# Kernel optimization log

Hardware: AMD Instinct MI355X
Metric: run time of the kernel (lower is better)

## Reference

```python
import jax, jax.numpy as jnp
import numpy as np

N, D_TOK, K = 8192, 256, 16


def knn_idx(xyz, k):
    # squared pairwise distances, diagonal excluded (loop=False)
    sq = jnp.sum(xyz * xyz, axis=-1)                      # [N]
    dist = sq[:, None] - 2.0 * (xyz @ xyz.T) + sq[None, :]  # [N,N]
    dist = dist + jnp.eye(xyz.shape[0], dtype=xyz.dtype) * jnp.asarray(1e10, xyz.dtype)
    _, idx = jax.lax.top_k(-dist, k)                      # [N,k] nearest neighbors j for each target i
    return idx


def edgeconv(x, nbr, W1, b1, W2, b2):
    # EdgeConv message: nn(concat(x_i, x_j - x_i)), aggr = max over neighbors
    n, d = x.shape
    k = nbr.shape[1]
    xi = x[:, None, :]                                    # [N,1,D]
    xj = x[nbr]                                           # [N,k,D] gather
    msg = jnp.concatenate([jnp.broadcast_to(xi, (n, k, d)), xj - xi], axis=-1)  # [N,k,2D]
    h = jax.nn.relu(msg @ W1 + b1) @ W2 + b2              # [N,k,token_dim]
    return jnp.max(h, axis=1)                             # [N,token_dim]


def setup_inputs() -> dict:
    key = jax.random.key(0)
    ks = jax.random.split(key, 10)
    d_in = 2 * (D_TOK + 3)
    s1 = 1.0 / np.sqrt(d_in)
    s2 = 1.0 / np.sqrt(D_TOK)
    return {
        "xyz": jax.random.normal(ks[0], (N, 3), dtype=jnp.float32),
        "feat": jax.random.normal(ks[1], (N, D_TOK), dtype=jnp.float32),
        "W1a": jax.random.normal(ks[2], (d_in, D_TOK), dtype=jnp.float32) * s1,
        "b1a": jnp.zeros((D_TOK,), dtype=jnp.float32),
        "W2a": jax.random.normal(ks[3], (D_TOK, D_TOK), dtype=jnp.float32) * s2,
        "b2a": jnp.zeros((D_TOK,), dtype=jnp.float32),
        "W1b": jax.random.normal(ks[4], (d_in, D_TOK), dtype=jnp.float32) * s1,
        "b1b": jnp.zeros((D_TOK,), dtype=jnp.float32),
        "W2b": jax.random.normal(ks[5], (D_TOK, D_TOK), dtype=jnp.float32) * s2,
        "b2b": jnp.zeros((D_TOK,), dtype=jnp.float32),
    }


def reference(xyz, feat, W1a, b1a, W2a, b2a, W1b, b1b, W2b, b2b):
    nbr = knn_idx(xyz, K)                                 # [N,k], built once, reused by both convs
    x = jnp.concatenate([feat, xyz], axis=-1)             # [N, D_TOK+3]
    x = edgeconv(x, nbr, W1a, b1a, W2a, b2a)              # [N, D_TOK]
    x = jnp.concatenate([x, xyz], axis=-1)                # [N, D_TOK+3]
    x = edgeconv(x, nbr, W1b, b1b, W2b, b2b)              # [N, D_TOK]
    return x
```

## Files before the change

### kernel.cpp

```cpp
#include <hip/hip_runtime.h>
#include <cfloat>

#define N_PTS 8192
#define DTOK 256
#define KNN 16

typedef __attribute__((ext_vector_type(8))) short short8;
typedef __attribute__((ext_vector_type(4))) float float4v;
typedef __attribute__((ext_vector_type(2))) float float2v;

__device__ inline short f2bf(float f) {
  unsigned u = __float_as_uint(f);
  u += 0x7fffu + ((u >> 16) & 1u);
  return (short)(u >> 16);
}
__device__ inline float bf2f(short h) {
  return __uint_as_float(((unsigned)(unsigned short)h) << 16);
}

__device__ inline float2v pk_mul(float2v a, float2v b) {
  float2v d;
  asm("v_pk_mul_f32 %0, %1, %2" : "=v"(d) : "v"(a), "v"(b));
  return d;
}
__device__ inline float2v pk_fma(float2v a, float2v b, float2v c) {
  float2v d;
  asm("v_pk_fma_f32 %0, %1, %2, %3" : "=v"(d) : "v"(a), "v"(b), "v"(c));
  return d;
}
__device__ inline float2v pk_add(float2v a, float2v b) {
  float2v d;
  asm("v_pk_add_f32 %0, %1, %2" : "=v"(d) : "v"(a), "v"(b));
  return d;
}

__global__ __launch_bounds__(256) void knn_prep_kernel(
    const float* __restrict__ xyz, float4* __restrict__ xyz4) {
  const int i = blockIdx.x * 256 + threadIdx.x;
  float x = xyz[3 * i], y = xyz[3 * i + 1], z = xyz[3 * i + 2];
  float sq = __fadd_rn(__fadd_rn(__fmul_rn(x, x), __fmul_rn(y, y)),
                       __fmul_rn(z, z));
  xyz4[i] = make_float4(x, y, z, sq);
}

__device__ inline void insert_group(float d, int base, float t, int lane,
                                    float& sd, int& sj, float& s15) {
  unsigned long long m = __ballot(d <= t);
  while (m) {
    const int src = __ffsll(m) - 1;
    m &= m - 1;
    const float dc = __shfl(d, src);
    if (dc < s15) {
      const int jc = base + src;
      const unsigned long long bm = __ballot(sd <= dc) & 0xFFFFull;
      const int pos = (int)__popcll(bm);
      const float pu = __shfl_up(sd, 1);
      const int ju = __shfl_up(sj, 1);
      if (lane < 16) {
        if (lane > pos)        { sd = pu; sj = ju; }
        else if (lane == pos)  { sd = dc; sj = jc; }
      }
      s15 = __shfl(sd, 15);
    }
  }
}

#define KCH 512
#define NCH (N_PTS / KCH)
#define QPW 4

__global__ __launch_bounds__(256) void knn_select_kernel(
    const float4* __restrict__ xyz4, int* __restrict__ nbr) {
  __shared__ float4 sA[2][4][64];
  __shared__ float4 sB[2][4][64];
  const int tid = threadIdx.x;
  const int lane = tid & 63;
  const int wave = tid >> 6;
  const int ibase = blockIdx.x * (4 * QPW) + wave * QPW;

  float2v qx[QPW], qy[QPW], qz[QPW], qs[QPW];
  #pragma unroll
  for (int q = 0; q < QPW; ++q) {
    const float4 p = xyz4[ibase + q];
    qx[q] = (float2v){p.x, p.x};
    qy[q] = (float2v){p.y, p.y};
    qz[q] = (float2v){p.z, p.z};
    qs[q] = (float2v){p.w, p.w};
  }
  const float2v n2 = {-2.0f, -2.0f};

  const int ib128 = ibase & ~127;
  int ihh[QPW], ill[QPW];
  #pragma unroll
  for (int q = 0; q < QPW; ++q) {
    ihh[q] = ((ibase + q) >> 6) & 1;
    ill[q] = (ibase + q) & 63;
  }

  const int sgj = wave * 128 + lane;

  {
    const float4 c0 = xyz4[sgj];
    const float4 c1 = xyz4[sgj + 64];
    sA[0][wave][lane] = make_float4(c0.x, c1.x, c0.y, c1.y);
    sB[0][wave][lane] = make_float4(c0.z, c1.z, c0.w, c1.w);
  }
  __syncthreads();

  float am0[QPW], am1[QPW];
  #pragma unroll
  for (int q = 0; q < QPW; ++q) { am0[q] = FLT_MAX; am1[q] = FLT_MAX; }

  for (int c = 0; c < NCH; ++c) {
    const int b = c & 1;
    float4 nx0, nx1;
    if (c < NCH - 1) {
      nx0 = xyz4[(c + 1) * KCH + sgj];
      nx1 = xyz4[(c + 1) * KCH + sgj + 64];
    }
    const int cbase = c * KCH;
    #pragma unroll
    for (int ps = 0; ps < 4; ++ps) {
      const float4 a = sA[b][ps][lane];
      const float4 bb = sB[b][ps][lane];
      const float2v px = {a.x, a.y}, py = {a.z, a.w};
      const float2v pz = {bb.x, bb.y}, pw = {bb.z, bb.w};
      const bool selfg = (cbase + ps * 128 == ib128);
      #pragma unroll
      for (int q = 0; q < QPW; ++q) {
        const float2v dot =
            pk_fma(qz[q], pz, pk_fma(qy[q], py, pk_mul(qx[q], px)));
        float2v d = pk_add(pk_fma(n2, dot, qs[q]), pw);
        if (selfg) {
          if (lane == ill[q]) {
            if (ihh[q]) d.y = __fadd_rn(d.y, 1e10f);
            else        d.x = __fadd_rn(d.x, 1e10f);
          }
        }
        am0[q] = fminf(am0[q], d.x);
        am1[q] = fminf(am1[q], d.y);
      }
    }
    if (c < NCH - 1) {
      sA[b ^ 1][wave][lane] = make_float4(nx0.x, nx1.x, nx0.y, nx1.y);
      sB[b ^ 1][wave][lane] = make_float4(nx0.z, nx1.z, nx0.w, nx1.w);
    }
    __syncthreads();
  }

  float v[QPW];
  #pragma unroll
  for (int q = 0; q < QPW; ++q) v[q] = fminf(am0[q], am1[q]);
  #pragma unroll
  for (int k = 2; k <= 64; k <<= 1) {
    #pragma unroll
    for (int j = k >> 1; j > 0; j >>= 1) {
      const bool keepmin = ((lane & k) == 0) == ((lane & j) == 0);
      #pragma unroll
      for (int q = 0; q < QPW; ++q) {
        const float o = __shfl_xor(v[q], j, 64);
        v[q] = keepmin ? fminf(v[q], o) : fmaxf(v[q], o);
      }
    }
  }
  float t[QPW];
  #pragma unroll
  for (int q = 0; q < QPW; ++q)
    t[q] = __shfl(v[q], 15, 64);

  float sd[QPW], s15[QPW];
  int sj[QPW];
  #pragma unroll
  for (int q = 0; q < QPW; ++q) {
    sd[q] = FLT_MAX; s15[q] = FLT_MAX; sj[q] = 0;
  }

  {
    const float4 c0 = xyz4[sgj];
    const float4 c1 = xyz4[sgj + 64];
    sA[0][wave][lane] = make_float4(c0.x, c1.x, c0.y, c1.y);
    sB[0][wave][lane] = make_float4(c0.z, c1.z, c0.w, c1.w);
  }
  __syncthreads();

  for (int c = 0; c < NCH; ++c) {
    const int b = c & 1;
    float4 nx0, nx1;
    if (c < NCH - 1) {
      nx0 = xyz4[(c + 1) * KCH + sgj];
      nx1 = xyz4[(c + 1) * KCH + sgj + 64];
    }
    const int cbase = c * KCH;

    #pragma unroll
    for (int ps = 0; ps < 4; ++ps) {
      const float4 a = sA[b][ps][lane];
      const float4 bb = sB[b][ps][lane];
      const float2v px = {a.x, a.y}, py = {a.z, a.w};
      const float2v pz = {bb.x, bb.y}, pw = {bb.z, bb.w};
      const int base = cbase + ps * 128;
      const bool selfg = (base == ib128);
      float2v dd[QPW];
      #pragma unroll
      for (int q = 0; q < QPW; ++q) {
        const float2v dot =
            pk_fma(qz[q], pz, pk_fma(qy[q], py, pk_mul(qx[q], px)));
        dd[q] = pk_add(pk_fma(n2, dot, qs[q]), pw);
        if (selfg) {
          if (lane == ill[q]) {
            if (ihh[q]) dd[q].y = __fadd_rn(dd[q].y, 1e10f);
            else        dd[q].x = __fadd_rn(dd[q].x, 1e10f);
          }
        }
      }
      #pragma unroll
      for (int q = 0; q < QPW; ++q) {
        insert_group(dd[q].x, base,      t[q], lane, sd[q], sj[q], s15[q]);
        insert_group(dd[q].y, base + 64, t[q], lane, sd[q], sj[q], s15[q]);
      }
    }

    if (c < NCH - 1) {
      sA[b ^ 1][wave][lane] = make_float4(nx0.x, nx1.x, nx0.y, nx1.y);
      sB[b ^ 1][wave][lane] = make_float4(nx0.z, nx1.z, nx0.w, nx1.w);
    }
    __syncthreads();
  }
  if (lane < 16) {
    #pragma unroll
    for (int q = 0; q < QPW; ++q)
      nbr[(ibase + q) * KNN + lane] = sj[q];
  }
}

__global__ __launch_bounds__(256) void convert_w_kernel(
    const float* __restrict__ W1, short* __restrict__ bhi,
    short* __restrict__ blo) {
  const int n = blockIdx.x;
  const int k = threadIdx.x;
  const float v = (n < 256) ? W1[k * DTOK + n]
                            : W1[(259 + k) * DTOK + (n - 256)];
  short h = f2bf(v);
  bhi[n * 256 + k] = h;
  blo[n * 256 + k] = f2bf(v - bf2f(h));
}

__global__ __launch_bounds__(256, 2) void pq_gemm_fused_kernel(
    const float* __restrict__ A, const short* __restrict__ Bthi,
    const short* __restrict__ Btlo, const float* __restrict__ xyz,
    const float* __restrict__ W1, const float* __restrict__ b1,
    float* __restrict__ R, float* __restrict__ Q) {
  __shared__ short Ahi[64][32], Alo[64][32];
  __shared__ short Bhi[128][32], Blo[128][32];
  __shared__ float Qs[64][65];
  __shared__ float sx[64][3];
  __shared__ float swz[6][64];
  __shared__ float sb1[64];

  const int tid = threadIdx.x;
  const int lane = tid & 63;
  const int wave = tid >> 6;
  const int l15 = lane & 15;
  const int quad = lane >> 4;
  const int mh = wave & 1;
  const int qh = wave >> 1;
  const int m0 = blockIdx.x * 64;
  const int np0 = blockIdx.y * 64;

  if (tid < 64) {
    sx[tid][0] = xyz[(m0 + tid) * 3];
    sx[tid][1] = xyz[(m0 + tid) * 3 + 1];
    sx[tid][2] = xyz[(m0 + tid) * 3 + 2];
  } else if (tid < 128) {
    int n = tid - 64;
    sb1[n] = b1[np0 + n];
    #pragma unroll
    for (int r = 0; r < 3; ++r) {
      swz[r][n] = W1[(256 + r) * DTOK + np0 + n];
      swz[3 + r][n] = W1[(515 + r) * DTOK + np0 + n];
    }
  }

  float4v acc[2][4];
  #pragma unroll
  for (int mf = 0; mf < 2; ++mf)
    #pragma unroll
    for (int nf = 0; nf < 4; ++nf)
      #pragma unroll
      for (int e = 0; e < 4; ++e) acc[mf][nf][e] = 0.f;

  const int ar = tid >> 2;
  const int ak = (tid & 3) * 8;

  #pragma unroll 1
  for (int kc = 0; kc < 8; ++kc) {
    const int k0 = kc * 32;
    __syncthreads();
    {
      const float* asrc = A + (size_t)(m0 + ar) * 256 + k0 + ak;
      float4 a0 = *(const float4*)asrc;
      float4 a1 = *(const float4*)(asrc + 4);
      float v[8] = {a0.x, a0.y, a0.z, a0.w, a1.x, a1.y, a1.z, a1.w};
      short8 h8, l8;
      #pragma unroll
      for (int e = 0; e < 8; ++e) {
        short h = f2bf(v[e]);
        h8[e] = h;
        l8[e] = f2bf(v[e] - bf2f(h));
      }
      *(short8*)(&Ahi[ar][ak]) = h8;
      *(short8*)(&Alo[ar][ak]) = l8;
    }
    #pragma unroll
    for (int l = 0; l < 4; ++l) {
      const int rem = tid + 256 * (l & 1);
      const int row = rem >> 2;
      const int koff = (rem & 3) * 8;
      const int n = (row < 64) ? (np0 + row) : (256 + np0 + row - 64);
      const short* src = ((l < 2) ? Bthi : Btlo) + (size_t)n * 256 + k0 + koff;
      short8 vv = *(const short8*)src;
      if (l < 2) *(short8*)(&Bhi[row][koff]) = vv;
      else       *(short8*)(&Blo[row][koff]) = vv;
    }
    __syncthreads();

    short8 ah[2], al[2], bh[4], bl[4];
    #pragma unroll
    for (int mf = 0; mf < 2; ++mf) {
      ah[mf] = *(const short8*)(&Ahi[mh * 32 + mf * 16 + l15][quad * 8]);
      al[mf] = *(const short8*)(&Alo[mh * 32 + mf * 16 + l15][quad * 8]);
    }
    #pragma unroll
    for (int nf = 0; nf < 4; ++nf) {
      bh[nf] = *(const short8*)(&Bhi[qh * 64 + nf * 16 + l15][quad * 8]);
      bl[nf] = *(const short8*)(&Blo[qh * 64 + nf * 16 + l15][quad * 8]);
    }
    #pragma unroll
    for (int mf = 0; mf < 2; ++mf)
      #pragma unroll
      for (int nf = 0; nf < 4; ++nf) {
        acc[mf][nf] = __builtin_amdgcn_mfma_f32_16x16x32_bf16(
            ah[mf], bh[nf], acc[mf][nf], 0, 0, 0);
        acc[mf][nf] = __builtin_amdgcn_mfma_f32_16x16x32_bf16(
            ah[mf], bl[nf], acc[mf][nf], 0, 0, 0);
        acc[mf][nf] = __builtin_amdgcn_mfma_f32_16x16x32_bf16(
            al[mf], bh[nf], acc[mf][nf], 0, 0, 0);
      }
  }

  if (qh == 1) {
    #pragma unroll
    for (int mf = 0; mf < 2; ++mf)
      #pragma unroll
      for (int nf = 0; nf < 4; ++nf)
        #pragma unroll
        for (int e = 0; e < 4; ++e) {
          int row = mh * 32 + mf * 16 + quad * 4 + e;
          int col = nf * 16 + l15;
          float q = acc[mf][nf][e] + sx[row][0] * swz[3][col] +
                    sx[row][1] * swz[4][col] + sx[row][2] * swz[5][col];
          Qs[row][col] = q;
          Q[(size_t)(m0 + row) * DTOK + np0 + col] = q;
        }
  }
  __syncthreads();
  if (qh == 0) {
    #pragma unroll
    for (int mf = 0; mf < 2; ++mf)
      #pragma unroll
      for (int nf = 0; nf < 4; ++nf)
        #pragma unroll
        for (int e = 0; e < 4; ++e) {
          int row = mh * 32 + mf * 16 + quad * 4 + e;
          int col = nf * 16 + l15;
          float p = acc[mf][nf][e] + sx[row][0] * swz[0][col] +
                    sx[row][1] * swz[1][col] + sx[row][2] * swz[2][col];
          R[(size_t)(m0 + row) * DTOK + np0 + col] =
              (p + sb1[col]) - Qs[row][col];
        }
  }
}

#define EP 8

__global__ __launch_bounds__(256, 2) void edge_mfma_kernel(
    const float* __restrict__ R, const float* __restrict__ Q,
    const int* __restrict__ nbr, const float* __restrict__ W2,
    const float* __restrict__ b2, float* __restrict__ out,
    int num_groups, int groups_per_block) {
  __shared__ short Hs[EP * KNN * DTOK];
  const int lane = threadIdx.x & 63;
  const int wave = threadIdx.x >> 6;
  const int l15 = lane & 15;
  const int quad = lane >> 4;

  short8 bfr[4][8];
  #pragma unroll
  for (int nt_i = 0; nt_i < 4; ++nt_i) {
    const int n = (wave * 4 + nt_i) * 16 + l15;
    #pragma unroll
    for (int kt = 0; kt < 8; ++kt) {
      short8 f;
      #pragma unroll
      for (int jj = 0; jj < 8; ++jj) {
        int k = kt * 32 + quad * 8 + jj;
        f[jj] = f2bf(W2[k * DTOK + n]);
      }
      bfr[nt_i][kt] = f;
    }
  }

  const int wc8 = lane >> 1;
  const int wsub = (lane & 1) * 4;

  for (int gi = 0; gi < groups_per_block; ++gi) {
    const int g = blockIdx.x + gi * gridDim.x;
    if (g >= num_groups) break;
    const int i0 = g * EP;

    {
      const int ia = i0 + wave * 2;
      const int jr0 = nbr[ia * KNN + l15];
      const int jr1 = nbr[(ia + 1) * KNN + l15];
      const float4 ri0 = ((const float4*)(R + (size_t)ia * DTOK))[lane];
      const float4 ri1 = ((const float4*)(R + (size_t)(ia + 1) * DTOK))[lane];
      #pragma unroll
      for (int pp = 0; pp < 2; ++pp) {
        const float4 ri = pp ? ri1 : ri0;
        const int jr = pp ? jr1 : jr0;
        #pragma unroll
        for (int k = 0; k < KNN; ++k) {
          const int j = __shfl(jr, k, 16);
          const float4 qj = ((const float4*)(Q + (size_t)j * DTOK))[lane];
          const int r = wave * 32 + pp * 16 + k;
          uint2 pk;
          pk.x = ((unsigned)(unsigned short)f2bf(fmaxf(ri.x + qj.x, 0.f))) |
                 (((unsigned)(unsigned short)f2bf(fmaxf(ri.y + qj.y, 0.f))) << 16);
          pk.y = ((unsigned)(unsigned short)f2bf(fmaxf(ri.z + qj.z, 0.f))) |
                 (((unsigned)(unsigned short)f2bf(fmaxf(ri.w + qj.w, 0.f))) << 16);
          *(uint2*)(&Hs[r * DTOK + ((wc8 ^ (r & 7)) << 3) + wsub]) = pk;
        }
      }
    }
    __syncthreads();

    #pragma unroll
    for (int mp = 0; mp < 4; ++mp) {
      float4v acc[2][4];
      #pragma unroll
      for (int mi = 0; mi < 2; ++mi)
        #pragma unroll
        for (int nt_i = 0; nt_i < 4; ++nt_i)
          #pragma unroll
          for (int e = 0; e < 4; ++e) acc[mi][nt_i][e] = 0.f;

      #pragma unroll
      for (int kt = 0; kt < 8; ++kt) {
        const int pc = ((kt * 4 + quad) ^ (l15 & 7)) << 3;
        const short8 a0 = *(const short8*)(
            &Hs[((mp * 2 + 0) * 16 + l15) * DTOK + pc]);
        const short8 a1 = *(const short8*)(
            &Hs[((mp * 2 + 1) * 16 + l15) * DTOK + pc]);
        #pragma unroll
        for (int nt_i = 0; nt_i < 4; ++nt_i) {
          acc[0][nt_i] = __builtin_amdgcn_mfma_f32_16x16x32_bf16(
              a0, bfr[nt_i][kt], acc[0][nt_i], 0, 0, 0);
          acc[1][nt_i] = __builtin_amdgcn_mfma_f32_16x16x32_bf16(
              a1, bfr[nt_i][kt], acc[1][nt_i], 0, 0, 0);
        }
      }

      #pragma unroll
      for (int mi = 0; mi < 2; ++mi) {
        #pragma unroll
        for (int nt_i = 0; nt_i < 4; ++nt_i) {
          float rm = fmaxf(fmaxf(acc[mi][nt_i][0], acc[mi][nt_i][1]),
                           fmaxf(acc[mi][nt_i][2], acc[mi][nt_i][3]));
          rm = fmaxf(rm, __shfl_xor(rm, 16, 64));
          rm = fmaxf(rm, __shfl_xor(rm, 32, 64));
          if (lane < 16) {
            const int i = i0 + mp * 2 + mi;
            const int n = (wave * 4 + nt_i) * 16 + lane;
            out[(size_t)i * DTOK + n] = rm + b2[n];
          }
        }
      }
    }
    __syncthreads();
  }
}

extern "C" void kernel_launch(void* const* d_in, const int* in_sizes, int n_in,
                              void* d_out, int out_size, void* d_ws,
                              size_t ws_size, hipStream_t stream) {
  const float* xyz = (const float*)d_in[0];
  const float* feat = (const float*)d_in[1];
  const float* W1a = (const float*)d_in[2];
  const float* b1a = (const float*)d_in[3];
  const float* W2a = (const float*)d_in[4];
  const float* b2a = (const float*)d_in[5];
  const float* W1b = (const float*)d_in[6];
  const float* b1b = (const float*)d_in[7];
  const float* W2b = (const float*)d_in[8];
  const float* b2b = (const float*)d_in[9];
  float* out = (float*)d_out;

  char* w = (char*)d_ws;
  const size_t SZ_NBR = (size_t)N_PTS * KNN * sizeof(int);
  const size_t MB = 1024 * 1024;
  int* nbr = (int*)w;
  char* w1 = w + SZ_NBR;
  float4* xyz4 = (float4*)w1;
  float* R = (float*)(w1 + 8 * MB);
  float* Q = (float*)(w + SZ_NBR + 16 * MB);
  short* Bthi = (short*)(w + SZ_NBR + 24 * MB);
  short* Btlo = Bthi + 512 * 256;
  float* bufC = out;

  knn_prep_kernel<<<N_PTS / 256, 256, 0, stream>>>(xyz, xyz4);
  knn_select_kernel<<<N_PTS / 16, 256, 0, stream>>>(xyz4, nbr);

  const int num_groups = N_PTS / EP;
  const int nblocks = 512;

  convert_w_kernel<<<512, 256, 0, stream>>>(W1a, Bthi, Btlo);
  pq_gemm_fused_kernel<<<dim3(N_PTS / 64, 4), 256, 0, stream>>>(
      feat, Bthi, Btlo, xyz, W1a, b1a, R, Q);
  edge_mfma_kernel<<<nblocks, 256, 0, stream>>>(R, Q, nbr, W2a, b2a, bufC,
                                                num_groups, 2);

  convert_w_kernel<<<512, 256, 0, stream>>>(W1b, Bthi, Btlo);
  pq_gemm_fused_kernel<<<dim3(N_PTS / 64, 4), 256, 0, stream>>>(
      bufC, Bthi, Btlo, xyz, W1b, b1b, R, Q);
  edge_mfma_kernel<<<nblocks, 256, 0, stream>>>(R, Q, nbr, W2b, b2b, out,
                                                num_groups, 2);
}
```

Before: 260.5 us.

## Split KNN candidate scan across two waves per query and merge top-16

The KNN select kernel now gives each group of 4 queries two waves, each scanning one half of the 8192 candidates. Each half builds its own threshold and its own top-16 list. The two lists are then merged in shared memory with a rank-based merge that breaks ties by half. The grid doubles to 1024 blocks, which is meant to raise occupancy and latency hiding on the select phase. In exchange, each block stages both halves in shared memory, adds an extra merge step with two more barriers, and each per-half threshold is looser than a threshold over all candidates.

```diff
diff --git a/kernel.cpp b/kernel.cpp
--- a/kernel.cpp
+++ b/kernel.cpp
@@ -65,22 +65,27 @@
   }
 }
 
-#define KCH 512
-#define NCH (N_PTS / KCH)
-#define QPW 4
+#define NST 8
 
 __global__ __launch_bounds__(256) void knn_select_kernel(
     const float4* __restrict__ xyz4, int* __restrict__ nbr) {
-  __shared__ float4 sA[2][4][64];
-  __shared__ float4 sB[2][4][64];
+  __shared__ float4 sA[2][2][4][64];
+  __shared__ float4 sB[2][2][4][64];
+  __shared__ float mgd[2][4][2][16];
+  __shared__ int   mgj[2][4][2][16];
+  __shared__ int   mo[8][16];
+
   const int tid = threadIdx.x;
   const int lane = tid & 63;
   const int wave = tid >> 6;
-  const int ibase = blockIdx.x * (4 * QPW) + wave * QPW;
-
-  float2v qx[QPW], qy[QPW], qz[QPW], qs[QPW];
-  #pragma unroll
-  for (int q = 0; q < QPW; ++q) {
+  const int g = wave >> 1;
+  const int h = wave & 1;
+  const int hbase = h * 4096;
+  const int ibase = blockIdx.x * 8 + g * 4;
+
+  float2v qx[4], qy[4], qz[4], qs[4];
+  #pragma unroll
+  for (int q = 0; q < 4; ++q) {
     const float4 p = xyz4[ibase + q];
     qx[q] = (float2v){p.x, p.x};
     qy[q] = (float2v){p.y, p.y};
@@ -89,45 +94,52 @@
   }
   const float2v n2 = {-2.0f, -2.0f};
 
-  const int ib128 = ibase & ~127;
-  int ihh[QPW], ill[QPW];
-  #pragma unroll
-  for (int q = 0; q < QPW; ++q) {
+  const int ib128 = (blockIdx.x * 8) & ~127;
+  const bool selfInHalf = ((ib128 >> 12) == h);
+  int ihh[4], ill[4];
+  #pragma unroll
+  for (int q = 0; q < 4; ++q) {
     ihh[q] = ((ibase + q) >> 6) & 1;
     ill[q] = (ibase + q) & 63;
   }
 
-  const int sgj = wave * 128 + lane;
+  const int soff = wave * 128 + lane;
 
   {
-    const float4 c0 = xyz4[sgj];
-    const float4 c1 = xyz4[sgj + 64];
-    sA[0][wave][lane] = make_float4(c0.x, c1.x, c0.y, c1.y);
-    sB[0][wave][lane] = make_float4(c0.z, c1.z, c0.w, c1.w);
+    const float4 c00 = xyz4[soff];
+    const float4 c01 = xyz4[soff + 64];
+    const float4 c10 = xyz4[4096 + soff];
+    const float4 c11 = xyz4[4096 + soff + 64];
+    sA[0][0][wave][lane] = make_float4(c00.x, c01.x, c00.y, c01.y);
+    sB[0][0][wave][lane] = make_float4(c00.z, c01.z, c00.w, c01.w);
+    sA[0][1][wave][lane] = make_float4(c10.x, c11.x, c10.y, c11.y);
+    sB[0][1][wave][lane] = make_float4(c10.z, c11.z, c10.w, c11.w);
   }
   __syncthreads();
 
-  float am0[QPW], am1[QPW];
-  #pragma unroll
-  for (int q = 0; q < QPW; ++q) { am0[q] = FLT_MAX; am1[q] = FLT_MAX; }
-
-  for (int c = 0; c < NCH; ++c) {
+  float am0[4], am1[4];
+  #pragma unroll
+  for (int q = 0; q < 4; ++q) { am0[q] = FLT_MAX; am1[q] = FLT_MAX; }
+
+  for (int c = 0; c < NST; ++c) {
     const int b = c & 1;
-    float4 nx0, nx1;
-    if (c < NCH - 1) {
-      nx0 = xyz4[(c + 1) * KCH + sgj];
-      nx1 = xyz4[(c + 1) * KCH + sgj + 64];
-    }
-    const int cbase = c * KCH;
+    float4 c00, c01, c10, c11;
+    if (c < NST - 1) {
+      c00 = xyz4[(c + 1) * 512 + soff];
+      c01 = xyz4[(c + 1) * 512 + soff + 64];
+      c10 = xyz4[4096 + (c + 1) * 512 + soff];
+      c11 = xyz4[4096 + (c + 1) * 512 + soff + 64];
+    }
+    const int cb = hbase + c * 512;
     #pragma unroll
     for (int ps = 0; ps < 4; ++ps) {
-      const float4 a = sA[b][ps][lane];
-      const float4 bb = sB[b][ps][lane];
+      const float4 a = sA[b][h][ps][lane];
+      const float4 bb = sB[b][h][ps][lane];
       const float2v px = {a.x, a.y}, py = {a.z, a.w};
       const float2v pz = {bb.x, bb.y}, pw = {bb.z, bb.w};
-      const bool selfg = (cbase + ps * 128 == ib128);
-      #pragma unroll
-      for (int q = 0; q < QPW; ++q) {
+      const bool selfg = selfInHalf && (cb + ps * 128 == ib128);
+      #pragma unroll
+      for (int q = 0; q < 4; ++q) {
         const float2v dot =
             pk_fma(qz[q], pz, pk_fma(qy[q], py, pk_mul(qx[q], px)));
         float2v d = pk_add(pk_fma(n2, dot, qs[q]), pw);
@@ -141,68 +153,73 @@
         am1[q] = fminf(am1[q], d.y);
       }
     }
-    if (c < NCH - 1) {
-      sA[b ^ 1][wave][lane] = make_float4(nx0.x, nx1.x, nx0.y, nx1.y);
-      sB[b ^ 1][wave][lane] = make_float4(nx0.z, nx1.z, nx0.w, nx1.w);
+    if (c < NST - 1) {
+      sA[b ^ 1][0][wave][lane] = make_float4(c00.x, c01.x, c00.y, c01.y);
+      sB[b ^ 1][0][wave][lane] = make_float4(c00.z, c01.z, c00.w, c01.w);
+      sA[b ^ 1][1][wave][lane] = make_float4(c10.x, c11.x, c10.y, c11.y);
+      sB[b ^ 1][1][wave][lane] = make_float4(c10.z, c11.z, c10.w, c11.w);
     }
     __syncthreads();
   }
 
-  float v[QPW];
-  #pragma unroll
-  for (int q = 0; q < QPW; ++q) v[q] = fminf(am0[q], am1[q]);
+  float4 p00 = xyz4[soff];
+  float4 p01 = xyz4[soff + 64];
+  float4 p10 = xyz4[4096 + soff];
+  float4 p11 = xyz4[4096 + soff + 64];
+
+  float v[4];
+  #pragma unroll
+  for (int q = 0; q < 4; ++q) v[q] = fminf(am0[q], am1[q]);
   #pragma unroll
   for (int k = 2; k <= 64; k <<= 1) {
     #pragma unroll
     for (int j = k >> 1; j > 0; j >>= 1) {
       const bool keepmin = ((lane & k) == 0) == ((lane & j) == 0);
       #pragma unroll
-      for (int q = 0; q < QPW; ++q) {
+      for (int q = 0; q < 4; ++q) {
         const float o = __shfl_xor(v[q], j, 64);
         v[q] = keepmin ? fminf(v[q], o) : fmaxf(v[q], o);
       }
     }
   }
-  float t[QPW];
-  #pragma unroll
-  for (int q = 0; q < QPW; ++q)
+  float t[4];
+  #pragma unroll
+  for (int q = 0; q < 4; ++q)
     t[q] = __shfl(v[q], 15, 64);
 
-  float sd[QPW], s15[QPW];
-  int sj[QPW];
-  #pragma unroll
-  for (int q = 0; q < QPW; ++q) {
-    sd[q] = FLT_MAX; s15[q] = FLT_MAX; sj[q] = 0;
-  }
-
-  {
-    const float4 c0 = xyz4[sgj];
-    const float4 c1 = xyz4[sgj + 64];
-    sA[0][wave][lane] = make_float4(c0.x, c1.x, c0.y, c1.y);
-    sB[0][wave][lane] = make_float4(c0.z, c1.z, c0.w, c1.w);
-  }
+  float sd[4], s15[4];
+  int sjv[4];
+  #pragma unroll
+  for (int q = 0; q < 4; ++q) { sd[q] = FLT_MAX; s15[q] = FLT_MAX; sjv[q] = 0; }
+
+  sA[0][0][wave][lane] = make_float4(p00.x, p01.x, p00.y, p01.y);
+  sB[0][0][wave][lane] = make_float4(p00.z, p01.z, p00.w, p01.w);
+  sA[0][1][wave][lane] = make_float4(p10.x, p11.x, p10.y, p11.y);
+  sB[0][1][wave][lane] = make_float4(p10.z, p11.z, p10.w, p11.w);
   __syncthreads();
 
-  for (int c = 0; c < NCH; ++c) {
+  for (int c = 0; c < NST; ++c) {
     const int b = c & 1;
-    float4 nx0, nx1;
-    if (c < NCH - 1) {
-      nx0 = xyz4[(c + 1) * KCH + sgj];
-      nx1 = xyz4[(c + 1) * KCH + sgj + 64];
-    }
-    const int cbase = c * KCH;
+    float4 c00, c01, c10, c11;
+    if (c < NST - 1) {
+      c00 = xyz4[(c + 1) * 512 + soff];
+      c01 = xyz4[(c + 1) * 512 + soff + 64];
+      c10 = xyz4[4096 + (c + 1) * 512 + soff];
+      c11 = xyz4[4096 + (c + 1) * 512 + soff + 64];
+    }
+    const int cb = hbase + c * 512;
 
     #pragma unroll
     for (int ps = 0; ps < 4; ++ps) {
-      const float4 a = sA[b][ps][lane];
-      const float4 bb = sB[b][ps][lane];
+      const float4 a = sA[b][h][ps][lane];
+      const float4 bb = sB[b][h][ps][lane];
       const float2v px = {a.x, a.y}, py = {a.z, a.w};
       const float2v pz = {bb.x, bb.y}, pw = {bb.z, bb.w};
-      const int base = cbase + ps * 128;
-      const bool selfg = (base == ib128);
-      float2v dd[QPW];
-      #pragma unroll
-      for (int q = 0; q < QPW; ++q) {
+      const int base = cb + ps * 128;
+      const bool selfg = selfInHalf && (base == ib128);
+      float2v dd[4];
+      #pragma unroll
+      for (int q = 0; q < 4; ++q) {
         const float2v dot =
             pk_fma(qz[q], pz, pk_fma(qy[q], py, pk_mul(qx[q], px)));
         dd[q] = pk_add(pk_fma(n2, dot, qs[q]), pw);
@@ -214,23 +231,50 @@
         }
       }
       #pragma unroll
-      for (int q = 0; q < QPW; ++q) {
-        insert_group(dd[q].x, base,      t[q], lane, sd[q], sj[q], s15[q]);
-        insert_group(dd[q].y, base + 64, t[q], lane, sd[q], sj[q], s15[q]);
-      }
-    }
-
-    if (c < NCH - 1) {
-      sA[b ^ 1][wave][lane] = make_float4(nx0.x, nx1.x, nx0.y, nx1.y);
-      sB[b ^ 1][wave][lane] = make_float4(nx0.z, nx1.z, nx0.w, nx1.w);
+      for (int q = 0; q < 4; ++q) {
+        insert_group(dd[q].x, base,      t[q], lane, sd[q], sjv[q], s15[q]);
+        insert_group(dd[q].y, base + 64, t[q], lane, sd[q], sjv[q], s15[q]);
+      }
+    }
+
+    if (c < NST - 1) {
+      sA[b ^ 1][0][wave][lane] = make_float4(c00.x, c01.x, c00.y, c01.y);
+      sB[b ^ 1][0][wave][lane] = make_float4(c00.z, c01.z, c00.w, c01.w);
+      sA[b ^ 1][1][wave][lane] = make_float4(c10.x, c11.x, c10.y, c11.y);
+      sB[b ^ 1][1][wave][lane] = make_float4(c10.z, c11.z, c10.w, c11.w);
     }
     __syncthreads();
   }
+
   if (lane < 16) {
     #pragma unroll
-    for (int q = 0; q < QPW; ++q)
-      nbr[(ibase + q) * KNN + lane] = sj[q];
-  }
+    for (int q = 0; q < 4; ++q) {
+      mgd[g][q][h][lane] = sd[q];
+      mgj[g][q][h][lane] = sjv[q];
+    }
+  }
+  __syncthreads();
+
+  {
+    const int qq = wave * 2 + (lane >> 5);
+    const int e = lane & 31;
+    const int L = e >> 4;
+    const int pos = e & 15;
+    const int mg_ = qq >> 2, mq = qq & 3;
+    const float de = mgd[mg_][mq][L][pos];
+    const int je = mgj[mg_][mq][L][pos];
+    int rank = pos;
+    #pragma unroll
+    for (int k = 0; k < 16; ++k) {
+      const float od = mgd[mg_][mq][L ^ 1][k];
+      rank += (L == 0) ? (od < de) : (od <= de);
+    }
+    if (rank < 16) mo[qq][rank] = je;
+  }
+  __syncthreads();
+
+  if (tid < 128)
+    nbr[(blockIdx.x * 8 + (tid >> 4)) * KNN + (tid & 15)] = mo[tid >> 4][tid & 15];
 }
 
 __global__ __launch_bounds__(256) void convert_w_kernel(
@@ -518,7 +562,7 @@
   float* bufC = out;
 
   knn_prep_kernel<<<N_PTS / 256, 256, 0, stream>>>(xyz, xyz4);
-  knn_select_kernel<<<N_PTS / 16, 256, 0, stream>>>(xyz4, nbr);
+  knn_select_kernel<<<N_PTS / 8, 256, 0, stream>>>(xyz4, nbr);
 
   const int num_groups = N_PTS / EP;
   const int nblocks = 512;
```

After: 279.1 us. 7.2% more time.
